# Performance work log

Hardware: AMD Instinct MI355X
Metric: run time of the kernel (lower is better)

## Reference

```python
import jax, jax.numpy as jnp
import numpy as np

KERNEL = (3, 3)
STRIDE = (1, 1)
# padding='zero', dimPadding='auto' -> pad = ceil((k-1)/2) per side on each dim
PAD = tuple(int(np.ceil((k - 1) / 2)) for k in KERNEL)


def setup_inputs() -> dict:
    key = jax.random.key(0)
    k1, k2 = jax.random.split(key)
    dataset = jax.random.normal(k1, (32, 64, 112, 112), dtype=jnp.float32)
    filters = jax.random.normal(k2, (128, 64, 3, 3), dtype=jnp.float32)
    return {"dataset": dataset, "filters": filters}


def reference(dataset, filters):
    # The torch module's unfold->multiply->sum->fold pipeline computes a plain
    # cross-correlation (conv2d) of NCHW input with OIHW filters, zero padding
    # PAD per side, stride STRIDE. Output: [B, F, Hout, Wout].
    out = jax.lax.conv_general_dilated(
        dataset, filters,
        window_strides=STRIDE,
        padding=((PAD[0], PAD[0]), (PAD[1], PAD[1])),
        dimension_numbers=("NCHW", "OIHW", "NCHW"),
    )
    return out
```

## Files before the change

kernel.cpp:

```cpp
#include <hip/hip_runtime.h>


typedef __attribute__((ext_vector_type(8))) __bf16 bf16x8;
typedef __attribute__((ext_vector_type(4))) float f32x4;
typedef __attribute__((ext_vector_type(4))) unsigned int u32x4;

#define XROW 7296
#define WPROW 120

__device__ __forceinline__ unsigned short f2bf(float f) {
    unsigned u = __builtin_bit_cast(unsigned, f);
    u += 0x7FFF + ((u >> 16) & 1);
    return (unsigned short)(u >> 16);
}

__device__ __forceinline__ void gload_lds16(const unsigned short* g, unsigned short* l) {
    __builtin_amdgcn_global_load_lds(
        (const __attribute__((address_space(1))) unsigned int*)g,
        (__attribute__((address_space(3))) unsigned int*)l, 16, 0, 0);
}

__global__ void prep_weights(const float* __restrict__ flt,
                             unsigned short* __restrict__ wsA) {
    int idx = blockIdx.x * 256 + threadIdx.x;
    if (idx >= 9 * 128 * 64) return;
    int off = idx >> 13;
    int f   = (idx >> 6) & 127;
    int c   = idx & 63;
    wsA[idx] = f2bf(flt[(f * 64 + c) * 9 + off]);
}

__global__ __launch_bounds__(512, 4)
void prep_input(const float* __restrict__ x, unsigned short* __restrict__ xt) {
    __shared__ __align__(16) unsigned short T[112 * 64];
    const int tid  = threadIdx.x;
    const int b    = blockIdx.x / 112;
    const int h    = blockIdx.x - b * 112;
    const int li   = tid & 7;
    const int unit = tid >> 3;

    for (int it = 0; it < 2; ++it) {
        int u = it * 64 + unit;
        if (u < 112) {
            int wo = u >> 3, cq = u & 7;
            int c  = cq * 8 + li;
            const float* src = x + (((size_t)b * 64 + c) * 112 + h) * 112 + wo * 8;
            f32x4 f0 = *(const f32x4*)src;
            f32x4 f1 = *(const f32x4*)(src + 4);
            float r[8] = {f0.x, f0.y, f0.z, f0.w, f1.x, f1.y, f1.z, f1.w};
#pragma unroll
            for (int d = 1; d < 8; d <<= 1) {
#pragma unroll
                for (int jA = 0; jA < 8; ++jA) {
                    if (jA & d) continue;
                    int jB = jA | d;
                    float give = (li & d) ? r[jA] : r[jB];
                    float got  = __shfl_xor(give, d, 64);
                    if (li & d) r[jA] = got; else r[jB] = got;
                }
            }
            unsigned pk[4];
#pragma unroll
            for (int j = 0; j < 4; ++j)
                pk[j] = (unsigned)f2bf(r[2 * j]) | ((unsigned)f2bf(r[2 * j + 1]) << 16);
            int w = wo * 8 + li;
            *(u32x4*)&T[w * 64 + (cq ^ (w & 7)) * 8] = u32x4{pk[0], pk[1], pk[2], pk[3]};
        }
    }
    __syncthreads();

    unsigned short* dst = xt + ((size_t)b * 114 + (h + 1)) * XROW;
    for (int ch = tid; ch < 912; ch += 512) {
        int wp = ch >> 3, cq = ch & 7;
        u32x4 v = {0, 0, 0, 0};
        if (wp >= 1 && wp <= 112) {
            int w = wp - 1;
            v = *(const u32x4*)&T[w * 64 + (cq ^ (w & 7)) * 8];
        }
        *(u32x4*)&dst[(size_t)ch * 8] = v;
    }
    if (h == 0 || h == 111) {
        unsigned short* zr = xt + ((size_t)b * 114 + (h == 0 ? 0 : 113)) * XROW;
        for (int ch = tid; ch < 912; ch += 512)
            *(u32x4*)&zr[(size_t)ch * 8] = u32x4{0, 0, 0, 0};
    }
}

template <int TW0, int NTW>
__device__ __forceinline__ void wave_kloop(const unsigned short* Bs,
                                           const unsigned short* wA,
                                           float* obase, int rr, int l16, int q) {
    f32x4 acc[4][NTW];
#pragma unroll
    for (int mt = 0; mt < 4; ++mt)
#pragma unroll
        for (int t = 0; t < NTW; ++t) acc[mt][t] = {0.f, 0.f, 0.f, 0.f};

#pragma unroll
    for (int off = 0; off < 9; ++off) {
        const int kh = off / 3;
        const int kw = off - kh * 3;
        const int rp = rr + kh;
#pragma unroll
        for (int cs = 0; cs < 2; ++cs) {
            bf16x8 a0 = *(const bf16x8*)(wA + off * 8192 + cs * 32);
            bf16x8 a1 = *(const bf16x8*)(wA + off * 8192 + 1024 + cs * 32);
            bf16x8 a2 = *(const bf16x8*)(wA + off * 8192 + 2048 + cs * 32);
            bf16x8 a3 = *(const bf16x8*)(wA + off * 8192 + 3072 + cs * 32);
            const int cq = cs * 4 + q;
#pragma unroll
            for (int t = 0; t < NTW; ++t) {
                int wp = (TW0 + t) * 16 + l16 + kw;
                int chunk = cq ^ (wp & 7);
                bf16x8 bv = *(const bf16x8*)&Bs[(rp * WPROW + wp) * 64 + chunk * 8];
                acc[0][t] = __builtin_amdgcn_mfma_f32_16x16x32_bf16(a0, bv, acc[0][t], 0, 0, 0);
                acc[1][t] = __builtin_amdgcn_mfma_f32_16x16x32_bf16(a1, bv, acc[1][t], 0, 0, 0);
                acc[2][t] = __builtin_amdgcn_mfma_f32_16x16x32_bf16(a2, bv, acc[2][t], 0, 0, 0);
                acc[3][t] = __builtin_amdgcn_mfma_f32_16x16x32_bf16(a3, bv, acc[3][t], 0, 0, 0);
            }
        }
    }
#pragma unroll
    for (int mt = 0; mt < 4; ++mt)
#pragma unroll
        for (int t = 0; t < NTW; ++t) {
            float* o = obase + (size_t)(mt * 16) * 12544 + (TW0 + t) * 16 + l16;
#pragma unroll
            for (int r2 = 0; r2 < 4; ++r2)
                o[(size_t)r2 * 12544] = acc[mt][t][r2];
        }
}

__global__ __launch_bounds__(512, 4)
void conv_fast(const unsigned short* __restrict__ xt,
               const unsigned short* __restrict__ wsA,
               float* __restrict__ out) {
    __shared__ __align__(16) unsigned short Bs[4 * WPROW * 64];

    const int tid = threadIdx.x;
    const int id  = blockIdx.x;
    const int xcd = id & 7;
    const int s   = id >> 3;
    const int b   = s / 7;
    const int hpl = s - b * 7;
    const int h0  = (xcd * 7 + hpl) * 2;

    const int lane = tid & 63;
    const int wid  = tid >> 6;

    {
        const unsigned short* xbase = xt + ((size_t)b * 114 + h0) * XROW;
        const int l3 = lane >> 3, j = lane & 7;
        for (int i = wid; i < 60; i += 8) {
            int rp  = i / 15;
            int seg = i - rp * 15;
            int wp  = seg * 8 + l3;
            int wps = wp <= 113 ? wp : 113;
            const unsigned short* src =
                xbase + (size_t)rp * XROW + wps * 64 + ((j ^ (wps & 7)) * 8);
            gload_lds16(src, &Bs[(rp * WPROW + seg * 8) * 64]);
        }
    }
    __syncthreads();

    const int l16 = lane & 15;
    const int q   = lane >> 4;
    const int fg  = wid & 1;
    const int rr  = (wid >> 1) & 1;
    const int ws  = wid >> 2;
    const int h   = h0 + rr;

    const unsigned short* wA = wsA + (fg * 64 + l16) * 64 + q * 8;
    float* obase = out + (((size_t)b * 128 + fg * 64 + q * 4) * 112 + h) * 112;

    if (ws == 0) wave_kloop<0, 4>(Bs, wA, obase, rr, l16, q);
    else         wave_kloop<4, 3>(Bs, wA, obase, rr, l16, q);
}

#define ROWS_PER_KH 124
#define ROW_SHORTS 64

__global__ __launch_bounds__(512, 4)
void conv_mfma(const float* __restrict__ x,
               const unsigned short* __restrict__ wsA,
               float* __restrict__ out) {
    __shared__ __align__(16) unsigned short Bso[4 * ROWS_PER_KH * ROW_SHORTS];

    const int tid = threadIdx.x;
    const int id  = blockIdx.x;
    const int xcd = id & 7;
    const int s   = id >> 3;
    const int b   = s / 7;
    const int hpl = s - b * 7;
    const int hp  = xcd * 7 + hpl;
    const int h0  = hp * 2;

    if (tid < 32) {
        int kh = tid >> 3, cq = tid & 7;
        int R = kh * ROWS_PER_KH;
        int chunk = cq ^ (R & 7);
        *(u32x4*)&Bso[R * ROW_SHORTS + chunk * 8] = u32x4{0, 0, 0, 0};
    }

    const int li   = tid & 7;
    const int unit = tid >> 3;
    for (int it = 0; it < 8; ++it) {
        int u = it * 64 + unit;
        if (u < 480) {
            int wo = u >> 5;
            int rc = u & 31;
            int rp = rc >> 3;
            int cq = rc & 7;
            int hr = h0 + rp - 1;
            int c  = cq * 8 + li;
            f32x4 f0 = {0.f, 0.f, 0.f, 0.f}, f1 = {0.f, 0.f, 0.f, 0.f};
            if ((unsigned)hr < 112u && wo < 14) {
                const float* src = x + (((size_t)b * 64 + c) * 112 + hr) * 112 + wo * 8;
                f0 = *(const f32x4*)src;
                f1 = *(const f32x4*)(src + 4);
            }
            float r[8] = {f0.x, f0.y, f0.z, f0.w, f1.x, f1.y, f1.z, f1.w};
#pragma unroll
            for (int d = 1; d < 8; d <<= 1) {
#pragma unroll
                for (int jA = 0; jA < 8; ++jA) {
                    if (jA & d) continue;
                    int jB = jA | d;
                    float give = (li & d) ? r[jA] : r[jB];
                    float got  = __shfl_xor(give, d, 64);
                    if (li & d) r[jA] = got; else r[jB] = got;
                }
            }
            int R = rp * ROWS_PER_KH + wo * 8 + li + 1;
            int chunk = cq ^ (R & 7);
            unsigned pk[4];
#pragma unroll
            for (int j = 0; j < 4; ++j)
                pk[j] = (unsigned)f2bf(r[2 * j]) | ((unsigned)f2bf(r[2 * j + 1]) << 16);
            *(u32x4*)&Bso[R * ROW_SHORTS + chunk * 8] = u32x4{pk[0], pk[1], pk[2], pk[3]};
        }
    }
    __syncthreads();

    const int lane = tid & 63;
    const int wid  = tid >> 6;
    const int fg   = wid & 3;
    const int rr   = wid >> 2;
    const int q    = lane >> 4;
    const int l16  = lane & 15;
    const int h    = h0 + rr;

    f32x4 acc[2][7];
#pragma unroll
    for (int mt = 0; mt < 2; ++mt)
#pragma unroll
        for (int tw = 0; tw < 7; ++tw)
            acc[mt][tw] = {0.f, 0.f, 0.f, 0.f};

    const unsigned short* wA = wsA + (fg * 32 + l16) * 64 + q * 8;

#pragma unroll
    for (int off = 0; off < 9; ++off) {
        const int kh = off / 3;
        const int kw = off - kh * 3;
        const int Rbase = (rr + kh) * ROWS_PER_KH + kw;
#pragma unroll
        for (int cs = 0; cs < 2; ++cs) {
            bf16x8 a0 = *(const bf16x8*)(wA + off * 8192 + cs * 32);
            bf16x8 a1 = *(const bf16x8*)(wA + off * 8192 + 1024 + cs * 32);
            const int cq = cs * 4 + q;
#pragma unroll
            for (int tw = 0; tw < 7; ++tw) {
                int R = Rbase + tw * 16 + l16;
                int chunk = cq ^ (R & 7);
                bf16x8 bv = *(const bf16x8*)&Bso[R * ROW_SHORTS + chunk * 8];
                acc[0][tw] = __builtin_amdgcn_mfma_f32_16x16x32_bf16(a0, bv, acc[0][tw], 0, 0, 0);
                acc[1][tw] = __builtin_amdgcn_mfma_f32_16x16x32_bf16(a1, bv, acc[1][tw], 0, 0, 0);
            }
        }
    }

#pragma unroll
    for (int mt = 0; mt < 2; ++mt) {
#pragma unroll
        for (int tw = 0; tw < 7; ++tw) {
            int f = fg * 32 + mt * 16 + q * 4;
            int w = tw * 16 + l16;
            float* o = out + (((size_t)b * 128 + f) * 112 + h) * 112 + w;
#pragma unroll
            for (int r2 = 0; r2 < 4; ++r2)
                o[(size_t)r2 * 12544] = acc[mt][tw][r2];
        }
    }
}

extern "C" void kernel_launch(void* const* d_in, const int* in_sizes, int n_in,
                              void* d_out, int out_size, void* d_ws, size_t ws_size,
                              hipStream_t stream) {
    const float* x   = (const float*)d_in[0];
    const float* flt = (const float*)d_in[1];
    float* out = (float*)d_out;
    unsigned short* wsA = (unsigned short*)d_ws;

    hipLaunchKernelGGL(prep_weights, dim3(288), dim3(256), 0, stream, flt, wsA);

    const size_t XT_BYTES = (size_t)32 * 114 * 114 * 64 * 2;
    const size_t need = 147456 + XT_BYTES;
    if (ws_size >= need) {
        unsigned short* xxt = wsA + 147456 / 2;
        hipLaunchKernelGGL(prep_input, dim3(3584), dim3(512), 0, stream, x, xxt);
        hipLaunchKernelGGL(conv_fast, dim3(1792), dim3(512), 0, stream, xxt, wsA, out);
    } else {
        hipLaunchKernelGGL(conv_mfma, dim3(1792), dim3(512), 0, stream, x, wsA, out);
    }
}
```

Before: 406.1 us.

## Stage swizzled weights in LDS and retile conv blocks to 4 rows × 64 filters

```diff
diff --git a/kernel.cpp b/kernel.cpp
--- a/kernel.cpp
+++ b/kernel.cpp
@@ -6,7 +6,7 @@
 typedef __attribute__((ext_vector_type(4))) unsigned int u32x4;
 
 #define XROW 7296
-#define WPROW 120
+#define WPROW 114
 
 __device__ __forceinline__ unsigned short f2bf(float f) {
     unsigned u = __builtin_bit_cast(unsigned, f);
@@ -19,15 +19,24 @@
         (const __attribute__((address_space(1))) unsigned int*)g,
         (__attribute__((address_space(3))) unsigned int*)l, 16, 0, 0);
 }
+__device__ __forceinline__ void gload_lds4(const unsigned short* g, unsigned short* l) {
+    __builtin_amdgcn_global_load_lds(
+        (const __attribute__((address_space(1))) unsigned int*)g,
+        (__attribute__((address_space(3))) unsigned int*)l, 4, 0, 0);
+}
 
 __global__ void prep_weights(const float* __restrict__ flt,
-                             unsigned short* __restrict__ wsA) {
+                             unsigned short* __restrict__ wsA,
+                             unsigned short* __restrict__ wsS) {
     int idx = blockIdx.x * 256 + threadIdx.x;
     if (idx >= 9 * 128 * 64) return;
     int off = idx >> 13;
     int f   = (idx >> 6) & 127;
     int c   = idx & 63;
-    wsA[idx] = f2bf(flt[(f * 64 + c) * 9 + off]);
+    unsigned short v = f2bf(flt[(f * 64 + c) * 9 + off]);
+    wsA[idx] = v;
+    int cq = c >> 3, cl = c & 7;
+    wsS[(off * 128 + f) * 64 + ((cq ^ (f & 7)) * 8 + cl)] = v;
 }
 
 __global__ __launch_bounds__(512, 4)
@@ -87,15 +96,16 @@
 }
 
 template <int TW0, int NTW>
-__device__ __forceinline__ void wave_kloop(const unsigned short* Bs,
-                                           const unsigned short* wA,
-                                           float* obase, int rr, int l16, int q) {
+__device__ __forceinline__ void kloop_lds(const unsigned short* Ws,
+                                          const unsigned short* Bs,
+                                          float* obase, int rr, int l16, int q) {
     f32x4 acc[4][NTW];
 #pragma unroll
     for (int mt = 0; mt < 4; ++mt)
 #pragma unroll
         for (int t = 0; t < NTW; ++t) acc[mt][t] = {0.f, 0.f, 0.f, 0.f};
 
+    const int e = l16 & 7;
 #pragma unroll
     for (int off = 0; off < 9; ++off) {
         const int kh = off / 3;
@@ -103,16 +113,17 @@
         const int rp = rr + kh;
 #pragma unroll
         for (int cs = 0; cs < 2; ++cs) {
-            bf16x8 a0 = *(const bf16x8*)(wA + off * 8192 + cs * 32);
-            bf16x8 a1 = *(const bf16x8*)(wA + off * 8192 + 1024 + cs * 32);
-            bf16x8 a2 = *(const bf16x8*)(wA + off * 8192 + 2048 + cs * 32);
-            bf16x8 a3 = *(const bf16x8*)(wA + off * 8192 + 3072 + cs * 32);
             const int cq = cs * 4 + q;
+            const int ca = cq ^ e;
+            bf16x8 a0 = *(const bf16x8*)&Ws[(off * 64 +      l16) * 64 + ca * 8];
+            bf16x8 a1 = *(const bf16x8*)&Ws[(off * 64 + 16 + l16) * 64 + ca * 8];
+            bf16x8 a2 = *(const bf16x8*)&Ws[(off * 64 + 32 + l16) * 64 + ca * 8];
+            bf16x8 a3 = *(const bf16x8*)&Ws[(off * 64 + 48 + l16) * 64 + ca * 8];
 #pragma unroll
             for (int t = 0; t < NTW; ++t) {
                 int wp = (TW0 + t) * 16 + l16 + kw;
-                int chunk = cq ^ (wp & 7);
-                bf16x8 bv = *(const bf16x8*)&Bs[(rp * WPROW + wp) * 64 + chunk * 8];
+                int cb = cq ^ (wp & 7);
+                bf16x8 bv = *(const bf16x8*)&Bs[(rp * WPROW + wp) * 64 + cb * 8];
                 acc[0][t] = __builtin_amdgcn_mfma_f32_16x16x32_bf16(a0, bv, acc[0][t], 0, 0, 0);
                 acc[1][t] = __builtin_amdgcn_mfma_f32_16x16x32_bf16(a1, bv, acc[1][t], 0, 0, 0);
                 acc[2][t] = __builtin_amdgcn_mfma_f32_16x16x32_bf16(a2, bv, acc[2][t], 0, 0, 0);
@@ -131,50 +142,62 @@
         }
 }
 
-__global__ __launch_bounds__(512, 4)
-void conv_fast(const unsigned short* __restrict__ xt,
-               const unsigned short* __restrict__ wsA,
-               float* __restrict__ out) {
-    __shared__ __align__(16) unsigned short Bs[4 * WPROW * 64];
+__global__ __launch_bounds__(512, 2)
+void conv_lds(const unsigned short* __restrict__ xt,
+              const unsigned short* __restrict__ wsS,
+              float* __restrict__ out) {
+    __shared__ __align__(16) unsigned short Ws[9 * 64 * 64];
+    __shared__ __align__(16) unsigned short Bs[6 * WPROW * 64];
 
     const int tid = threadIdx.x;
     const int id  = blockIdx.x;
     const int xcd = id & 7;
     const int s   = id >> 3;
     const int b   = s / 7;
-    const int hpl = s - b * 7;
-    const int h0  = (xcd * 7 + hpl) * 2;
+    const int u   = s - b * 7;
+    const int ix  = xcd * 7 + u;
+    const int fg  = ix & 1;
+    const int quad = ix >> 1;
 
     const int lane = tid & 63;
     const int wid  = tid >> 6;
 
+    const unsigned short* xrow = xt + ((size_t)b * 114 + quad * 4) * XROW;
     {
-        const unsigned short* xbase = xt + ((size_t)b * 114 + h0) * XROW;
         const int l3 = lane >> 3, j = lane & 7;
-        for (int i = wid; i < 60; i += 8) {
-            int rp  = i / 15;
-            int seg = i - rp * 15;
-            int wp  = seg * 8 + l3;
-            int wps = wp <= 113 ? wp : 113;
-            const unsigned short* src =
-                xbase + (size_t)rp * XROW + wps * 64 + ((j ^ (wps & 7)) * 8);
-            gload_lds16(src, &Bs[(rp * WPROW + seg * 8) * 64]);
+        for (int i = wid; i < 156; i += 8) {
+            if (i < 72) {
+                int off = i >> 3, k = i & 7;
+                gload_lds16(wsS + off * 8192 + fg * 4096 + k * 512 + lane * 8,
+                            &Ws[off * 4096 + k * 512]);
+            } else {
+                int i2 = i - 72;
+                int rp = i2 / 14, seg = i2 - rp * 14;
+                int wp = seg * 8 + l3;
+                gload_lds16(xrow + (size_t)rp * XROW + wp * 64 + ((j ^ (wp & 7)) * 8),
+                            &Bs[(rp * WPROW + seg * 8) * 64]);
+            }
+        }
+        if (wid < 6) {
+            int rp = wid;
+            int wp = 112 + (lane >> 5);
+            int cq = (lane & 31) >> 2;
+            gload_lds4(xrow + (size_t)rp * XROW + wp * 64 + (cq ^ (wp & 7)) * 8 + (lane & 3) * 2,
+                       &Bs[(rp * WPROW + 112) * 64]);
         }
     }
     __syncthreads();
 
     const int l16 = lane & 15;
     const int q   = lane >> 4;
-    const int fg  = wid & 1;
-    const int rr  = (wid >> 1) & 1;
+    const int rr  = wid & 3;
     const int ws  = wid >> 2;
-    const int h   = h0 + rr;
-
-    const unsigned short* wA = wsA + (fg * 64 + l16) * 64 + q * 8;
+    const int h   = quad * 4 + rr;
+
     float* obase = out + (((size_t)b * 128 + fg * 64 + q * 4) * 112 + h) * 112;
 
-    if (ws == 0) wave_kloop<0, 4>(Bs, wA, obase, rr, l16, q);
-    else         wave_kloop<4, 3>(Bs, wA, obase, rr, l16, q);
+    if (ws == 0) kloop_lds<0, 4>(Ws, Bs, obase, rr, l16, q);
+    else         kloop_lds<4, 3>(Ws, Bs, obase, rr, l16, q);
 }
 
 #define ROWS_PER_KH 124
@@ -301,15 +324,16 @@
     const float* flt = (const float*)d_in[1];
     float* out = (float*)d_out;
     unsigned short* wsA = (unsigned short*)d_ws;
-
-    hipLaunchKernelGGL(prep_weights, dim3(288), dim3(256), 0, stream, flt, wsA);
-
-    const size_t XT_BYTES = (size_t)32 * 114 * 114 * 64 * 2;
-    const size_t need = 147456 + XT_BYTES;
+    unsigned short* wsS = wsA + 73728;
+    unsigned short* xxt = wsA + 147456;
+
+    hipLaunchKernelGGL(prep_weights, dim3(288), dim3(256), 0, stream, flt, wsA, wsS);
+
+    const size_t XT_SHORTS = (size_t)32 * 114 * 114 * 64;
+    const size_t need = (147456 + XT_SHORTS) * 2;
     if (ws_size >= need) {
-        unsigned short* xxt = wsA + 147456 / 2;
         hipLaunchKernelGGL(prep_input, dim3(3584), dim3(512), 0, stream, x, xxt);
-        hipLaunchKernelGGL(conv_fast, dim3(1792), dim3(512), 0, stream, xxt, wsA, out);
+        hipLaunchKernelGGL(conv_lds, dim3(1792), dim3(512), 0, stream, xxt, wsS, out);
     } else {
         hipLaunchKernelGGL(conv_mfma, dim3(1792), dim3(512), 0, stream, x, wsA, out);
     }
```

Result: faster. 344.8 us (-15.1%).
